# Kernel optimization log

Measured on AMD Instinct MI355X. Metric: run time of the kernel, lower is better.

Reference implementation:

```python
import jax, jax.numpy as jnp
import numpy as np

N, K, C, CL = 1024, 32, 64, 128
H = 2 * C  # MLP hidden = 2 * pair channels


def _ln(x, g, b, eps=1e-5):
    m = x.mean(-1, keepdims=True)
    v = jnp.mean(jnp.square(x - m), -1, keepdims=True)
    return (x - m) * jax.lax.rsqrt(v + eps) * g + b


def setup_inputs() -> dict:
    key = jax.random.key(0)
    ks = jax.random.split(key, 16)

    def w(k, shape):
        return jax.random.normal(k, shape, jnp.float32) / np.float32(np.sqrt(shape[0]))

    local = jax.random.normal(ks[0], (N, CL), jnp.float32)
    pair = jax.random.normal(ks[1], (N, N, C), jnp.float32)
    pair_update = jax.random.normal(ks[2], (N, K, C), jnp.float32)
    r = jax.random.randint(ks[3], (N, K), -(N // 4), N)
    neighbours = jnp.where(r < 0, -1, r)
    mask = jax.random.bernoulli(ks[4], 0.9, (N,))
    return dict(
        local=local, pair=pair, pair_update=pair_update,
        neighbours=neighbours, mask=mask,
        Wa=w(ks[5], (CL, C)), Wb=w(ks[6], (CL, C)),
        ln_g=jnp.ones((C,), jnp.float32), ln_b=jnp.zeros((C,), jnp.float32),
        W_aug=w(ks[7], (C, C)), W_lin=w(ks[8], (C, C)),
        W_left=w(ks[9], (C, 32)), b_left=jnp.zeros((32,), jnp.float32),
        W_right=w(ks[10], (C, 32)), b_right=jnp.zeros((32,), jnp.float32),
        W1=w(ks[11], (32, H)), W2=w(ks[12], (H, C)),
        W_int=w(ks[13], (CL, C)), b_int=jnp.zeros((C,), jnp.float32),
    )


def reference(local, pair, pair_update, neighbours, mask,
              Wa, Wb, ln_g, ln_b, W_aug, W_lin,
              W_left, b_left, W_right, b_right, W1, W2, W_int, b_int):
    idx = jnp.arange(pair.shape[0])
    # inject local info into the sparse pair update   [N,K,C]
    pu = pair_update + (local @ Wa)[:, None] + (local @ Wb)[neighbours]
    # gather neighbour pair features + layernorm      [N,K,C]
    lp = _ln(pair[idx[:, None], neighbours], ln_g, ln_b)
    lp = lp + pu @ W_aug
    linear = lp @ W_lin                               # [N,K,C]
    left = lp @ W_left + b_left                       # [N,K,32]
    right = lp @ W_right + b_right                    # [N,K,32]
    # neighbour-of-neighbour pair features            [N,K,K,32]
    npair = left[:, None] + right[neighbours]
    pn = neighbours[neighbours]                       # [N,K,K]
    pn = jnp.where((neighbours == -1)[:, :, None], pn, -1)
    pm = (pn != -1) & mask[pn] & (neighbours != -1)[:, None, :]
    # fused per-edge-pair MLP                          [N,K,K,C]
    upd = jax.nn.gelu(npair @ W1) @ W2
    # masked mean over the middle neighbour axis       [N,K,C]
    upd = jnp.where(pm[..., None], upd, 0.0).sum(axis=1)
    upd = upd / jnp.maximum(pm.sum(axis=1), 1).astype(upd.dtype)[..., None]
    inter = local @ W_int + b_int                     # [N,C]
    # scatter-add back into the dense pair tensor (collisions possible)
    return pair.at[idx[:, None], neighbours].add(upd + inter[:, None] + linear)
```

## Files before the change

### kernel.cpp

```cpp
#include <hip/hip_runtime.h>
#include <hip/hip_bf16.h>

constexpr int Nn  = 1024;
constexpr int Kk  = 32;
constexpr int Cc  = 64;
constexpr int CLl = 128;

typedef unsigned int   u32;
typedef unsigned short u16;

__device__ __forceinline__ float gelu_tanh(float v){
  float c = 0.7978845608028654f*(v + 0.044715f*v*v*v);
  return 0.5f*v*(1.f + tanhf(c));
}
__device__ __forceinline__ float bflo(u32 u){ return __uint_as_float(u<<16); }
__device__ __forceinline__ float bfhi(u32 u){ return __uint_as_float(u & 0xffff0000u); }
__device__ __forceinline__ u32 pack_bf(float a, float b){
  u32 xa = __float_as_uint(a), xb = __float_as_uint(b);
  u32 ra = (xa + 0x7fffu + ((xa>>16)&1u)) >> 16;
  u32 rb = (xb + 0x7fffu + ((xb>>16)&1u)) >> 16;
  return ra | (rb<<16);
}

__global__ __launch_bounds__(64) void k0(
    const float* __restrict__ local, const float* __restrict__ Wa,
    const float* __restrict__ Wb, const float* __restrict__ Wint,
    const float* __restrict__ b_int,
    float* __restrict__ A, float* __restrict__ B, float* __restrict__ inter){
  int i = blockIdx.x;
  int c = threadIdx.x;
  __shared__ float l[CLl];
  l[c]      = local[i*CLl + c];
  l[c + 64] = local[i*CLl + 64 + c];
  __syncthreads();
  float a = 0.f, b = 0.f, t = 0.f;
  #pragma unroll 4
  for(int d = 0; d < CLl; ++d){
    float ld = l[d];
    a = fmaf(ld, Wa[d*Cc + c], a);
    b = fmaf(ld, Wb[d*Cc + c], b);
    t = fmaf(ld, Wint[d*Cc + c], t);
  }
  A[i*Cc + c] = a;
  B[i*Cc + c] = b;
  inter[i*Cc + c] = t + b_int[c];
}

__global__ __launch_bounds__(256) void k1(
    const float* __restrict__ pair, const float* __restrict__ pair_update,
    const int* __restrict__ neigh, const int* __restrict__ mask,
    const float* __restrict__ ln_g, const float* __restrict__ ln_b,
    const float* __restrict__ W_aug, const float* __restrict__ W_right,
    const float* __restrict__ b_right,
    const float* __restrict__ A, const float* __restrict__ B,
    float* __restrict__ r1023, int* __restrict__ qpart){
  const int i = Nn - 1;
  __shared__ float wA[4096];
  __shared__ float wR[2048];
  __shared__ float p [Kk][68];
  __shared__ float pu[Kk][68];
  __shared__ float lp[Kk][68];
  __shared__ int   nwS[Kk];
  __shared__ float ssum[Kk][9], ssq[Kk][9], stats[Kk][2];
  int tid = threadIdx.x;
  for(int idx = tid; idx < 4096; idx += 256) wA[idx] = W_aug[idx];
  for(int idx = tid; idx < 2048; idx += 256) wR[idx] = W_right[idx];
  if(tid < Kk){
    int n = neigh[i*Kk + tid];
    nwS[tid] = (n < 0) ? n + Nn : n;
    qpart[tid] = (n != -1 && mask[n] != 0) ? 1 : 0;
  }
  __syncthreads();
  int k = tid >> 3, s = tid & 7;
  {
    const float* prow = pair + ((size_t)i*Nn + nwS[k])*Cc + s*8;
    const float* pur  = pair_update + ((size_t)i*Kk + k)*Cc + s*8;
    const float* Ar = A + i*Cc + s*8;
    const float* Br = B + (size_t)nwS[k]*Cc + s*8;
    float ps = 0.f, ps2 = 0.f;
    for(int j = 0; j < 8; ++j){
      float v = prow[j];
      p[k][s*8 + j] = v; ps += v; ps2 += v*v;
      pu[k][s*8 + j] = pur[j] + Ar[j] + Br[j];
    }
    ssum[k][s] = ps; ssq[k][s] = ps2;
  }
  __syncthreads();
  if(s == 0){
    float m = 0.f, q = 0.f;
    for(int j = 0; j < 8; ++j){ m += ssum[k][j]; q += ssq[k][j]; }
    m *= (1.f/64.f); q *= (1.f/64.f);
    float var = fmaxf(q - m*m, 0.f);
    stats[k][0] = m; stats[k][1] = rsqrtf(var + 1e-5f);
  }
  __syncthreads();
  {
    float m = stats[k][0], r = stats[k][1];
    float acc[8];
    #pragma unroll
    for(int j = 0; j < 8; ++j){
      int c = s*8 + j;
      acc[j] = (p[k][c] - m)*r*ln_g[c] + ln_b[c];
    }
    for(int d = 0; d < 64; ++d){
      float pd = pu[k][d];
      #pragma unroll
      for(int j = 0; j < 8; ++j) acc[j] = fmaf(pd, wA[d*64 + s*8 + j], acc[j]);
    }
    #pragma unroll
    for(int j = 0; j < 8; ++j) lp[k][s*8 + j] = acc[j];
  }
  __syncthreads();
  {
    float acc[4] = {0.f,0.f,0.f,0.f};
    for(int d = 0; d < 64; ++d){
      float ld = lp[k][d];
      #pragma unroll
      for(int j = 0; j < 4; ++j) acc[j] = fmaf(ld, wR[d*32 + s*4 + j], acc[j]);
    }
    #pragma unroll
    for(int j = 0; j < 4; ++j)
      r1023[k*32 + s*4 + j] = acc[j] + b_right[s*4 + j];
  }
}

__global__ __launch_bounds__(256) void k2a(
    const float* __restrict__ pair, const float* __restrict__ pair_update,
    const int* __restrict__ neigh,
    const float* __restrict__ ln_g, const float* __restrict__ ln_b,
    const float* __restrict__ W_aug, const float* __restrict__ W_lin,
    const float* __restrict__ W_left, const float* __restrict__ b_left,
    const float* __restrict__ A, const float* __restrict__ B,
    const float* __restrict__ inter, const float* __restrict__ r1023,
    float* __restrict__ hG, float* __restrict__ linG){
  __shared__ u32 wbA[2048];
  __shared__ u32 wbL[2048];
  __shared__ u32 wbF[1024];
  __shared__ float pbuf [Kk][68];
  __shared__ float pubuf[Kk][68];
  __shared__ float AiS[64], InS[64], lgS[64], lbS[64];
  __shared__ float ssum[Kk][9], ssq[Kk][9], stats[Kk][2];
  __shared__ int nwS[Kk];

  int i   = blockIdx.x;
  int tid = threadIdx.x;

  for(int idx = tid; idx < 2048; idx += 256){
    const float2 wa = *(const float2*)(W_aug + idx*2);
    wbA[idx] = pack_bf(wa.x, wa.y);
    const float2 wl = *(const float2*)(W_lin + idx*2);
    wbL[idx] = pack_bf(wl.x, wl.y);
  }
  for(int idx = tid; idx < 1024; idx += 256){
    const float2 wf = *(const float2*)(W_left + idx*2);
    wbF[idx] = pack_bf(wf.x, wf.y);
  }
  if(tid < Kk){
    int n = neigh[i*Kk + tid];
    nwS[tid] = (n < 0) ? n + Nn : n;
  }
  if(tid < 64){
    AiS[tid] = A[i*Cc + tid];
    InS[tid] = inter[i*Cc + tid];
    lgS[tid] = ln_g[tid];
    lbS[tid] = ln_b[tid];
  }
  __syncthreads();

  {
    int k8 = tid >> 3, s8 = tid & 7;
    const float4* p4 = (const float4*)(pair + ((size_t)i*Nn + nwS[k8])*Cc) + s8*2;
    float4 p0 = p4[0], p1 = p4[1];
    const float4* u4 = (const float4*)(pair_update + ((size_t)i*Kk + k8)*Cc) + s8*2;
    float4 u0 = u4[0], u1 = u4[1];
    const float4* Br = (const float4*)(B + (size_t)nwS[k8]*Cc) + s8*2;
    float4 b0 = Br[0], b1 = Br[1];
    float pf[8] = {p0.x,p0.y,p0.z,p0.w,p1.x,p1.y,p1.z,p1.w};
    float uf[8] = {u0.x,u0.y,u0.z,u0.w,u1.x,u1.y,u1.z,u1.w};
    float bv[8] = {b0.x,b0.y,b0.z,b0.w,b1.x,b1.y,b1.z,b1.w};
    float ps = 0.f, ps2 = 0.f;
    #pragma unroll
    for(int j = 0; j < 8; ++j){
      float v = pf[j];
      pbuf[k8][s8*8 + j] = v; ps += v; ps2 += v*v;
      pubuf[k8][s8*8 + j] = uf[j] + AiS[s8*8 + j] + bv[j];
    }
    ssum[k8][s8] = ps; ssq[k8][s8] = ps2;
  }
  __syncthreads();

  if((tid & 7) == 0){
    int k8 = tid >> 3;
    float m = 0.f, q = 0.f;
    for(int j = 0; j < 8; ++j){ m += ssum[k8][j]; q += ssq[k8][j]; }
    m *= (1.f/64.f); q *= (1.f/64.f);
    float var = fmaxf(q - m*m, 0.f);
    stats[k8][0] = m; stats[k8][1] = rsqrtf(var + 1e-5f);
  }
  __syncthreads();

  int kq = tid >> 4;
  int s  = tid & 15;
  int k0 = kq, k1i = kq + 16;
  int c0 = s*4;

  float a0[4], a1[4];
  {
    float m0 = stats[k0][0], r0 = stats[k0][1];
    float m1 = stats[k1i][0], r1 = stats[k1i][1];
    #pragma unroll
    for(int j = 0; j < 4; ++j){
      int c = c0 + j;
      a0[j] = (pbuf[k0][c]  - m0)*r0*lgS[c] + lbS[c];
      a1[j] = (pbuf[k1i][c] - m1)*r1*lgS[c] + lbS[c];
    }
    #pragma unroll 4
    for(int d = 0; d < 64; ++d){
      uint2 wv = *(const uint2*)&wbA[d*32 + s*2];
      float w0 = bflo(wv.x), w1 = bfhi(wv.x), w2 = bflo(wv.y), w3 = bfhi(wv.y);
      float p0 = pubuf[k0][d], p1 = pubuf[k1i][d];
      a0[0] = fmaf(p0, w0, a0[0]); a0[1] = fmaf(p0, w1, a0[1]);
      a0[2] = fmaf(p0, w2, a0[2]); a0[3] = fmaf(p0, w3, a0[3]);
      a1[0] = fmaf(p1, w0, a1[0]); a1[1] = fmaf(p1, w1, a1[1]);
      a1[2] = fmaf(p1, w2, a1[2]); a1[3] = fmaf(p1, w3, a1[3]);
    }
  }
  __syncthreads();
  {
    #pragma unroll
    for(int j = 0; j < 4; ++j){ pbuf[k0][c0 + j] = a0[j]; pbuf[k1i][c0 + j] = a1[j]; }
  }
  __syncthreads();

  {
    float L0[4] = {0,0,0,0}, L1[4] = {0,0,0,0};
    float X0[2] = {0,0},     X1[2] = {0,0};
    #pragma unroll 4
    for(int d = 0; d < 64; ++d){
      float p0 = pbuf[k0][d], p1 = pbuf[k1i][d];
      uint2 wv = *(const uint2*)&wbL[d*32 + s*2];
      float w0 = bflo(wv.x), w1 = bfhi(wv.x), w2 = bflo(wv.y), w3 = bfhi(wv.y);
      L0[0] = fmaf(p0, w0, L0[0]); L0[1] = fmaf(p0, w1, L0[1]);
      L0[2] = fmaf(p0, w2, L0[2]); L0[3] = fmaf(p0, w3, L0[3]);
      L1[0] = fmaf(p1, w0, L1[0]); L1[1] = fmaf(p1, w1, L1[1]);
      L1[2] = fmaf(p1, w2, L1[2]); L1[3] = fmaf(p1, w3, L1[3]);
      u32 wf = wbF[d*16 + s];
      float f0 = bflo(wf), f1 = bfhi(wf);
      X0[0] = fmaf(p0, f0, X0[0]); X0[1] = fmaf(p0, f1, X0[1]);
      X1[0] = fmaf(p1, f0, X1[0]); X1[1] = fmaf(p1, f1, X1[1]);
    }
    float4 o0 = make_float4(L0[0]+InS[c0], L0[1]+InS[c0+1], L0[2]+InS[c0+2], L0[3]+InS[c0+3]);
    float4 o1 = make_float4(L1[0]+InS[c0], L1[1]+InS[c0+1], L1[2]+InS[c0+2], L1[3]+InS[c0+3]);
    *(float4*)(linG + ((size_t)i*Kk + k0 )*Cc + c0) = o0;
    *(float4*)(linG + ((size_t)i*Kk + k1i)*Cc + c0) = o1;
    int x0 = s*2;
    float2 bl = *(const float2*)(b_left + x0);
    float2 rA = *(const float2*)(r1023 + k0*32  + x0);
    float2 rB = *(const float2*)(r1023 + k1i*32 + x0);
    float2 h0 = make_float2(X0[0] + bl.x + rA.x, X0[1] + bl.y + rA.y);
    float2 h1 = make_float2(X1[0] + bl.x + rB.x, X1[1] + bl.y + rB.y);
    *(float2*)(hG + ((size_t)i*Kk + k0 )*32 + x0) = h0;
    *(float2*)(hG + ((size_t)i*Kk + k1i)*32 + x0) = h1;
  }
}

__global__ __launch_bounds__(256) void kfuse(
    const float* __restrict__ pair, const int* __restrict__ neigh,
    const float* __restrict__ W1, const float* __restrict__ W2,
    const float* __restrict__ hG, const float* __restrict__ linG,
    const int* __restrict__ qpart,
    float* __restrict__ out){
  __shared__ u32 w1b[2048];
  __shared__ u32 w2b[4096];
  __shared__ float hbuf[Kk][36];
  __shared__ float cbuf[Kk][68];
  __shared__ int nbS[Kk], nwS[Kk], quS[Kk], leadS[Kk];
  __shared__ int cminus;

  int i   = blockIdx.x;
  int tid = threadIdx.x;

  {
    const float4* src = (const float4*)(pair + (size_t)i*Nn*Cc);
    float4*       dst = (float4*)(out + (size_t)i*Nn*Cc);
    #pragma unroll 4
    for(int idx = tid; idx < 16384; idx += 256) dst[idx] = src[idx];
  }

  for(int idx = tid; idx < 2048; idx += 256){
    const float2 w1 = *(const float2*)(W1 + idx*2);
    w1b[idx] = pack_bf(w1.x, w1.y);
    const float2 wa = *(const float2*)(W2 + idx*2);
    w2b[idx] = pack_bf(wa.x, wa.y);
    const float2 wb2 = *(const float2*)(W2 + 4096 + idx*2);
    w2b[2048 + idx] = pack_bf(wb2.x, wb2.y);
  }
  for(int idx = tid; idx < 1024; idx += 256)
    hbuf[idx >> 5][idx & 31] = hG[(size_t)i*1024 + idx];
  if(tid < Kk){
    int n = neigh[i*Kk + tid];
    nbS[tid] = n;
    nwS[tid] = (n < 0) ? n + Nn : n;
    quS[tid] = qpart[tid];
  }
  __syncthreads();
  if(tid == 0){
    int c = 0;
    for(int kk = 0; kk < Kk; ++kk) c |= (nbS[kk] == -1);
    cminus = c;
  }

  int kq = tid >> 4;
  int s  = tid & 15;

  float g0[8], g1v[8];
  {
    float A0[8], A1[8];
    #pragma unroll
    for(int j = 0; j < 8; ++j){ A0[j] = 0.f; A1[j] = 0.f; }
    #pragma unroll 2
    for(int x = 0; x < 32; ++x){
      float h0 = hbuf[kq][x], h1 = hbuf[kq+16][x];
      uint4 wv = *(const uint4*)&w1b[x*64 + s*4];
      float w[8] = {bflo(wv.x),bfhi(wv.x),bflo(wv.y),bfhi(wv.y),
                    bflo(wv.z),bfhi(wv.z),bflo(wv.w),bfhi(wv.w)};
      #pragma unroll
      for(int j = 0; j < 8; ++j){
        A0[j] = fmaf(h0, w[j], A0[j]);
        A1[j] = fmaf(h1, w[j], A1[j]);
      }
    }
    #pragma unroll
    for(int j = 0; j < 8; ++j){ g0[j] = gelu_tanh(A0[j]); g1v[j] = gelu_tanh(A1[j]); }
  }
  __syncthreads();

  {
    float V0[4] = {0,0,0,0}, V1[4] = {0,0,0,0};
    int lbase = (kq & 3) << 4;
    for(int hb = 0; hb < 16; ++hb){
      int src = lbase | hb;
      #pragma unroll
      for(int hj = 0; hj < 8; ++hj){
        float gA = __shfl(g0[hj],  src, 64);
        float gB = __shfl(g1v[hj], src, 64);
        int h = hb*8 + hj;
        uint2 wv = *(const uint2*)&w2b[h*32 + s*2];
        float w0 = bflo(wv.x), w1 = bfhi(wv.x), w2 = bflo(wv.y), w3 = bfhi(wv.y);
        V0[0] = fmaf(gA, w0, V0[0]); V0[1] = fmaf(gA, w1, V0[1]);
        V0[2] = fmaf(gA, w2, V0[2]); V0[3] = fmaf(gA, w3, V0[3]);
        V1[0] = fmaf(gB, w0, V1[0]); V1[1] = fmaf(gB, w1, V1[1]);
        V1[2] = fmaf(gB, w2, V1[2]); V1[3] = fmaf(gB, w3, V1[3]);
      }
    }
    int c0 = s*4;
    float4 l0 = *(const float4*)(linG + ((size_t)i*Kk + kq     )*Cc + c0);
    float4 l1 = *(const float4*)(linG + ((size_t)i*Kk + kq + 16)*Cc + c0);
    float mul0 = (cminus && quS[kq]      && nbS[kq]      != -1) ? 1.f : 0.f;
    float mul1 = (cminus && quS[kq + 16] && nbS[kq + 16] != -1) ? 1.f : 0.f;
    cbuf[kq][c0+0] = fmaf(mul0, V0[0], l0.x);
    cbuf[kq][c0+1] = fmaf(mul0, V0[1], l0.y);
    cbuf[kq][c0+2] = fmaf(mul0, V0[2], l0.z);
    cbuf[kq][c0+3] = fmaf(mul0, V0[3], l0.w);
    cbuf[kq+16][c0+0] = fmaf(mul1, V1[0], l1.x);
    cbuf[kq+16][c0+1] = fmaf(mul1, V1[1], l1.y);
    cbuf[kq+16][c0+2] = fmaf(mul1, V1[2], l1.z);
    cbuf[kq+16][c0+3] = fmaf(mul1, V1[3], l1.w);
  }
  __syncthreads();

  if(tid < Kk){
    int lead = 1;
    for(int kk = 0; kk < tid; ++kk) if(nwS[kk] == nwS[tid]) lead = 0;
    leadS[tid] = lead;
  }
  __syncthreads();
  {
    int k8 = tid >> 3, s8 = tid & 7;
    if(leadS[k8]){
      int col = nwS[k8];
      float tot[8] = {0,0,0,0,0,0,0,0};
      for(int kk = 0; kk < Kk; ++kk){
        if(nwS[kk] == col){
          #pragma unroll
          for(int j = 0; j < 8; ++j) tot[j] += cbuf[kk][s8*8 + j];
        }
      }
      size_t base = ((size_t)i*Nn + col)*Cc + s8*8;
      const float4* pv = (const float4*)(pair + base);
      float4 p0 = pv[0], p1 = pv[1];
      float4 o0 = make_float4(p0.x+tot[0], p0.y+tot[1], p0.z+tot[2], p0.w+tot[3]);
      float4 o1 = make_float4(p1.x+tot[4], p1.y+tot[5], p1.z+tot[6], p1.w+tot[7]);
      float4* ov = (float4*)(out + base);
      ov[0] = o0; ov[1] = o1;
    }
  }
}

extern "C" void kernel_launch(void* const* d_in, const int* in_sizes, int n_in,
                              void* d_out, int out_size, void* d_ws, size_t ws_size,
                              hipStream_t stream){
  (void)in_sizes; (void)n_in; (void)out_size; (void)ws_size;
  const float* local       = (const float*)d_in[0];
  const float* pair        = (const float*)d_in[1];
  const float* pair_update = (const float*)d_in[2];
  const int*   neighbours  = (const int*)d_in[3];
  const int*   mask        = (const int*)d_in[4];
  const float* Wa          = (const float*)d_in[5];
  const float* Wb          = (const float*)d_in[6];
  const float* ln_g        = (const float*)d_in[7];
  const float* ln_b        = (const float*)d_in[8];
  const float* W_aug       = (const float*)d_in[9];
  const float* W_lin       = (const float*)d_in[10];
  const float* W_left      = (const float*)d_in[11];
  const float* b_left      = (const float*)d_in[12];
  const float* W_right     = (const float*)d_in[13];
  const float* b_right     = (const float*)d_in[14];
  const float* W1          = (const float*)d_in[15];
  const float* W2          = (const float*)d_in[16];
  const float* W_int       = (const float*)d_in[17];
  const float* b_int       = (const float*)d_in[18];

  float* ws    = (float*)d_ws;
  float* A     = ws;
  float* B     = ws + 65536;
  float* inter = ws + 131072;
  float* r1023 = ws + 196608;
  int*   qpart = (int*)(ws + 197632);
  float* hG    = ws + 197664;
  float* linG  = ws + 1246240;

  k0<<<dim3(Nn), dim3(64), 0, stream>>>(local, Wa, Wb, W_int, b_int, A, B, inter);
  k1<<<dim3(1), dim3(256), 0, stream>>>(pair, pair_update, neighbours, mask,
                                        ln_g, ln_b, W_aug, W_right, b_right,
                                        A, B, r1023, qpart);
  k2a<<<dim3(Nn), dim3(256), 0, stream>>>(pair, pair_update, neighbours,
                                          ln_g, ln_b, W_aug, W_lin, W_left, b_left,
                                          A, B, inter, r1023, hG, linG);
  kfuse<<<dim3(Nn), dim3(256), 0, stream>>>(pair, neighbours, W1, W2, hG, linG,
                                            qpart, (float*)d_out);
}
```

Baseline: 548.7 us.

## Fuse k2a and kfuse into one kernel with interleaved row copy

Merges the per-row projection kernel and the MLP/scatter kernel into a single kernel, keeping h and linear in registers and shared memory instead of passing them through global workspace buffers. The dense pair-to-out row copy is split into three chunks placed between compute phases so memory traffic can overlap with arithmetic. The pair_update sum is also stored as packed bf16 in shared memory. Shared-memory use rises, which can lower occupancy, and the bf16 packing of the input activation adds precision loss.

```diff
diff --git a/kernel.cpp b/kernel.cpp
--- a/kernel.cpp
+++ b/kernel.cpp
@@ -8,6 +8,7 @@
 
 typedef unsigned int   u32;
 typedef unsigned short u16;
+typedef float f4v __attribute__((ext_vector_type(4)));
 
 __device__ __forceinline__ float gelu_tanh(float v){
   float c = 0.7978845608028654f*(v + 0.044715f*v*v*v);
@@ -124,32 +125,58 @@
   }
 }
 
-__global__ __launch_bounds__(256) void k2a(
+__global__ __launch_bounds__(256) void kbig(
     const float* __restrict__ pair, const float* __restrict__ pair_update,
     const int* __restrict__ neigh,
     const float* __restrict__ ln_g, const float* __restrict__ ln_b,
     const float* __restrict__ W_aug, const float* __restrict__ W_lin,
     const float* __restrict__ W_left, const float* __restrict__ b_left,
+    const float* __restrict__ W1, const float* __restrict__ W2,
     const float* __restrict__ A, const float* __restrict__ B,
     const float* __restrict__ inter, const float* __restrict__ r1023,
-    float* __restrict__ hG, float* __restrict__ linG){
+    const int* __restrict__ qpart,
+    float* __restrict__ out){
+
   __shared__ u32 wbA[2048];
   __shared__ u32 wbL[2048];
   __shared__ u32 wbF[1024];
-  __shared__ float pbuf [Kk][68];
-  __shared__ float pubuf[Kk][68];
+  __shared__ u32 w1b[2048];
+  __shared__ u32 w2b[4096];
+  __shared__ float pbuf[Kk][68];
+  __shared__ u32  puP [Kk][34];
+  __shared__ float uA[1088];
+  __shared__ float stats[Kk][2];
   __shared__ float AiS[64], InS[64], lgS[64], lbS[64];
-  __shared__ float ssum[Kk][9], ssq[Kk][9], stats[Kk][2];
-  __shared__ int nwS[Kk];
-
-  int i   = blockIdx.x;
-  int tid = threadIdx.x;
+  __shared__ int nbS[Kk], nwS[Kk], quS[Kk], leadS[Kk];
+  __shared__ int cminus;
+
+  float* ssum = uA;
+  float* ssq  = uA + 288;
+  float* hbuf = uA;
+
+  const int i   = blockIdx.x;
+  const int tid = threadIdx.x;
+
+  const f4v* __restrict__ srcRow = (const f4v*)(pair + (size_t)i*Nn*Cc);
+  f4v* __restrict__       dstRow = (f4v*)(out + (size_t)i*Nn*Cc);
+
+  #pragma unroll 4
+  for(int it = 0; it < 32; ++it){
+    int idx = it*256 + tid;
+    dstRow[idx] = srcRow[idx];
+  }
 
   for(int idx = tid; idx < 2048; idx += 256){
     const float2 wa = *(const float2*)(W_aug + idx*2);
     wbA[idx] = pack_bf(wa.x, wa.y);
     const float2 wl = *(const float2*)(W_lin + idx*2);
     wbL[idx] = pack_bf(wl.x, wl.y);
+    const float2 w1 = *(const float2*)(W1 + idx*2);
+    w1b[idx] = pack_bf(w1.x, w1.y);
+    const float2 w2a = *(const float2*)(W2 + idx*2);
+    w2b[idx] = pack_bf(w2a.x, w2a.y);
+    const float2 w2c = *(const float2*)(W2 + 4096 + idx*2);
+    w2b[2048 + idx] = pack_bf(w2c.x, w2c.y);
   }
   for(int idx = tid; idx < 1024; idx += 256){
     const float2 wf = *(const float2*)(W_left + idx*2);
@@ -157,7 +184,9 @@
   }
   if(tid < Kk){
     int n = neigh[i*Kk + tid];
+    nbS[tid] = n;
     nwS[tid] = (n < 0) ? n + Nn : n;
+    quS[tid] = qpart[tid];
   }
   if(tid < 64){
     AiS[tid] = A[i*Cc + tid];
@@ -166,6 +195,17 @@
     lbS[tid] = ln_b[tid];
   }
   __syncthreads();
+
+  if(tid == 0){
+    int c = 0;
+    for(int kk = 0; kk < Kk; ++kk) c |= (nbS[kk] == -1);
+    cminus = c;
+  }
+  if(tid < Kk){
+    int lead = 1;
+    for(int kk = 0; kk < tid; ++kk) if(nwS[kk] == nwS[tid]) lead = 0;
+    leadS[tid] = lead;
+  }
 
   {
     int k8 = tid >> 3, s8 = tid & 7;
@@ -183,144 +223,117 @@
     for(int j = 0; j < 8; ++j){
       float v = pf[j];
       pbuf[k8][s8*8 + j] = v; ps += v; ps2 += v*v;
-      pubuf[k8][s8*8 + j] = uf[j] + AiS[s8*8 + j] + bv[j];
-    }
-    ssum[k8][s8] = ps; ssq[k8][s8] = ps2;
+    }
+    #pragma unroll
+    for(int j = 0; j < 4; ++j){
+      float e0 = uf[2*j]   + AiS[s8*8 + 2*j]   + bv[2*j];
+      float e1 = uf[2*j+1] + AiS[s8*8 + 2*j+1] + bv[2*j+1];
+      puP[k8][s8*4 + j] = pack_bf(e0, e1);
+    }
+    ssum[k8*9 + s8] = ps; ssq[k8*9 + s8] = ps2;
   }
   __syncthreads();
 
   if((tid & 7) == 0){
     int k8 = tid >> 3;
     float m = 0.f, q = 0.f;
-    for(int j = 0; j < 8; ++j){ m += ssum[k8][j]; q += ssq[k8][j]; }
+    for(int j = 0; j < 8; ++j){ m += ssum[k8*9 + j]; q += ssq[k8*9 + j]; }
     m *= (1.f/64.f); q *= (1.f/64.f);
     float var = fmaxf(q - m*m, 0.f);
     stats[k8][0] = m; stats[k8][1] = rsqrtf(var + 1e-5f);
   }
   __syncthreads();
 
-  int kq = tid >> 4;
-  int s  = tid & 15;
-  int k0 = kq, k1i = kq + 16;
-  int c0 = s*4;
+  const int kq  = tid >> 4;
+  const int s   = tid & 15;
+  const int k0i = kq, k1i = kq + 16;
+  const int c0  = s*4;
 
   float a0[4], a1[4];
   {
-    float m0 = stats[k0][0], r0 = stats[k0][1];
+    float m0 = stats[k0i][0], r0 = stats[k0i][1];
     float m1 = stats[k1i][0], r1 = stats[k1i][1];
     #pragma unroll
     for(int j = 0; j < 4; ++j){
       int c = c0 + j;
-      a0[j] = (pbuf[k0][c]  - m0)*r0*lgS[c] + lbS[c];
+      a0[j] = (pbuf[k0i][c] - m0)*r0*lgS[c] + lbS[c];
       a1[j] = (pbuf[k1i][c] - m1)*r1*lgS[c] + lbS[c];
     }
+    #pragma unroll 2
+    for(int dp = 0; dp < 32; ++dp){
+      u32 q0 = puP[k0i][dp], q1 = puP[k1i][dp];
+      float pe0 = bflo(q0), po0 = bfhi(q0);
+      float pe1 = bflo(q1), po1 = bfhi(q1);
+      uint2 we = *(const uint2*)&wbA[(2*dp)*32 + s*2];
+      uint2 wo = *(const uint2*)&wbA[(2*dp+1)*32 + s*2];
+      float w0 = bflo(we.x), w1 = bfhi(we.x), w2 = bflo(we.y), w3 = bfhi(we.y);
+      a0[0] = fmaf(pe0, w0, a0[0]); a0[1] = fmaf(pe0, w1, a0[1]);
+      a0[2] = fmaf(pe0, w2, a0[2]); a0[3] = fmaf(pe0, w3, a0[3]);
+      a1[0] = fmaf(pe1, w0, a1[0]); a1[1] = fmaf(pe1, w1, a1[1]);
+      a1[2] = fmaf(pe1, w2, a1[2]); a1[3] = fmaf(pe1, w3, a1[3]);
+      float x0w = bflo(wo.x), x1w = bfhi(wo.x), x2w = bflo(wo.y), x3w = bfhi(wo.y);
+      a0[0] = fmaf(po0, x0w, a0[0]); a0[1] = fmaf(po0, x1w, a0[1]);
+      a0[2] = fmaf(po0, x2w, a0[2]); a0[3] = fmaf(po0, x3w, a0[3]);
+      a1[0] = fmaf(po1, x0w, a1[0]); a1[1] = fmaf(po1, x1w, a1[1]);
+      a1[2] = fmaf(po1, x2w, a1[2]); a1[3] = fmaf(po1, x3w, a1[3]);
+    }
+  }
+  __syncthreads();
+  #pragma unroll
+  for(int j = 0; j < 4; ++j){ pbuf[k0i][c0 + j] = a0[j]; pbuf[k1i][c0 + j] = a1[j]; }
+
+  #pragma unroll 4
+  for(int it = 32; it < 48; ++it){
+    int idx = it*256 + tid;
+    dstRow[idx] = srcRow[idx];
+  }
+  __syncthreads();
+
+  float L0[4], L1[4];
+  {
+    float Lx0[4] = {0,0,0,0}, Lx1[4] = {0,0,0,0};
+    float X0[2] = {0,0}, X1[2] = {0,0};
     #pragma unroll 4
     for(int d = 0; d < 64; ++d){
-      uint2 wv = *(const uint2*)&wbA[d*32 + s*2];
-      float w0 = bflo(wv.x), w1 = bfhi(wv.x), w2 = bflo(wv.y), w3 = bfhi(wv.y);
-      float p0 = pubuf[k0][d], p1 = pubuf[k1i][d];
-      a0[0] = fmaf(p0, w0, a0[0]); a0[1] = fmaf(p0, w1, a0[1]);
-      a0[2] = fmaf(p0, w2, a0[2]); a0[3] = fmaf(p0, w3, a0[3]);
-      a1[0] = fmaf(p1, w0, a1[0]); a1[1] = fmaf(p1, w1, a1[1]);
-      a1[2] = fmaf(p1, w2, a1[2]); a1[3] = fmaf(p1, w3, a1[3]);
-    }
-  }
-  __syncthreads();
-  {
-    #pragma unroll
-    for(int j = 0; j < 4; ++j){ pbuf[k0][c0 + j] = a0[j]; pbuf[k1i][c0 + j] = a1[j]; }
-  }
-  __syncthreads();
-
-  {
-    float L0[4] = {0,0,0,0}, L1[4] = {0,0,0,0};
-    float X0[2] = {0,0},     X1[2] = {0,0};
-    #pragma unroll 4
-    for(int d = 0; d < 64; ++d){
-      float p0 = pbuf[k0][d], p1 = pbuf[k1i][d];
+      float p0 = pbuf[k0i][d], p1 = pbuf[k1i][d];
       uint2 wv = *(const uint2*)&wbL[d*32 + s*2];
       float w0 = bflo(wv.x), w1 = bfhi(wv.x), w2 = bflo(wv.y), w3 = bfhi(wv.y);
-      L0[0] = fmaf(p0, w0, L0[0]); L0[1] = fmaf(p0, w1, L0[1]);
-      L0[2] = fmaf(p0, w2, L0[2]); L0[3] = fmaf(p0, w3, L0[3]);
-      L1[0] = fmaf(p1, w0, L1[0]); L1[1] = fmaf(p1, w1, L1[1]);
-      L1[2] = fmaf(p1, w2, L1[2]); L1[3] = fmaf(p1, w3, L1[3]);
+      Lx0[0] = fmaf(p0, w0, Lx0[0]); Lx0[1] = fmaf(p0, w1, Lx0[1]);
+      Lx0[2] = fmaf(p0, w2, Lx0[2]); Lx0[3] = fmaf(p0, w3, Lx0[3]);
+      Lx1[0] = fmaf(p1, w0, Lx1[0]); Lx1[1] = fmaf(p1, w1, Lx1[1]);
+      Lx1[2] = fmaf(p1, w2, Lx1[2]); Lx1[3] = fmaf(p1, w3, Lx1[3]);
       u32 wf = wbF[d*16 + s];
       float f0 = bflo(wf), f1 = bfhi(wf);
       X0[0] = fmaf(p0, f0, X0[0]); X0[1] = fmaf(p0, f1, X0[1]);
       X1[0] = fmaf(p1, f0, X1[0]); X1[1] = fmaf(p1, f1, X1[1]);
     }
-    float4 o0 = make_float4(L0[0]+InS[c0], L0[1]+InS[c0+1], L0[2]+InS[c0+2], L0[3]+InS[c0+3]);
-    float4 o1 = make_float4(L1[0]+InS[c0], L1[1]+InS[c0+1], L1[2]+InS[c0+2], L1[3]+InS[c0+3]);
-    *(float4*)(linG + ((size_t)i*Kk + k0 )*Cc + c0) = o0;
-    *(float4*)(linG + ((size_t)i*Kk + k1i)*Cc + c0) = o1;
+    #pragma unroll
+    for(int j = 0; j < 4; ++j){
+      L0[j] = Lx0[j] + InS[c0 + j];
+      L1[j] = Lx1[j] + InS[c0 + j];
+    }
     int x0 = s*2;
     float2 bl = *(const float2*)(b_left + x0);
-    float2 rA = *(const float2*)(r1023 + k0*32  + x0);
+    float2 rA = *(const float2*)(r1023 + k0i*32 + x0);
     float2 rB = *(const float2*)(r1023 + k1i*32 + x0);
-    float2 h0 = make_float2(X0[0] + bl.x + rA.x, X0[1] + bl.y + rA.y);
-    float2 h1 = make_float2(X1[0] + bl.x + rB.x, X1[1] + bl.y + rB.y);
-    *(float2*)(hG + ((size_t)i*Kk + k0 )*32 + x0) = h0;
-    *(float2*)(hG + ((size_t)i*Kk + k1i)*32 + x0) = h1;
-  }
-}
-
-__global__ __launch_bounds__(256) void kfuse(
-    const float* __restrict__ pair, const int* __restrict__ neigh,
-    const float* __restrict__ W1, const float* __restrict__ W2,
-    const float* __restrict__ hG, const float* __restrict__ linG,
-    const int* __restrict__ qpart,
-    float* __restrict__ out){
-  __shared__ u32 w1b[2048];
-  __shared__ u32 w2b[4096];
-  __shared__ float hbuf[Kk][36];
-  __shared__ float cbuf[Kk][68];
-  __shared__ int nbS[Kk], nwS[Kk], quS[Kk], leadS[Kk];
-  __shared__ int cminus;
-
-  int i   = blockIdx.x;
-  int tid = threadIdx.x;
-
-  {
-    const float4* src = (const float4*)(pair + (size_t)i*Nn*Cc);
-    float4*       dst = (float4*)(out + (size_t)i*Nn*Cc);
-    #pragma unroll 4
-    for(int idx = tid; idx < 16384; idx += 256) dst[idx] = src[idx];
-  }
-
-  for(int idx = tid; idx < 2048; idx += 256){
-    const float2 w1 = *(const float2*)(W1 + idx*2);
-    w1b[idx] = pack_bf(w1.x, w1.y);
-    const float2 wa = *(const float2*)(W2 + idx*2);
-    w2b[idx] = pack_bf(wa.x, wa.y);
-    const float2 wb2 = *(const float2*)(W2 + 4096 + idx*2);
-    w2b[2048 + idx] = pack_bf(wb2.x, wb2.y);
-  }
-  for(int idx = tid; idx < 1024; idx += 256)
-    hbuf[idx >> 5][idx & 31] = hG[(size_t)i*1024 + idx];
-  if(tid < Kk){
-    int n = neigh[i*Kk + tid];
-    nbS[tid] = n;
-    nwS[tid] = (n < 0) ? n + Nn : n;
-    quS[tid] = qpart[tid];
-  }
-  __syncthreads();
-  if(tid == 0){
-    int c = 0;
-    for(int kk = 0; kk < Kk; ++kk) c |= (nbS[kk] == -1);
-    cminus = c;
-  }
-
-  int kq = tid >> 4;
-  int s  = tid & 15;
+    hbuf[k0i*34 + x0]     = X0[0] + bl.x + rA.x;
+    hbuf[k0i*34 + x0 + 1] = X0[1] + bl.y + rA.y;
+    hbuf[k1i*34 + x0]     = X1[0] + bl.x + rB.x;
+    hbuf[k1i*34 + x0 + 1] = X1[1] + bl.y + rB.y;
+  }
+  #pragma unroll 4
+  for(int it = 48; it < 64; ++it){
+    int idx = it*256 + tid;
+    dstRow[idx] = srcRow[idx];
+  }
+  __syncthreads();
 
   float g0[8], g1v[8];
   {
-    float A0[8], A1[8];
-    #pragma unroll
-    for(int j = 0; j < 8; ++j){ A0[j] = 0.f; A1[j] = 0.f; }
+    float A0[8] = {0,0,0,0,0,0,0,0}, A1[8] = {0,0,0,0,0,0,0,0};
     #pragma unroll 2
     for(int x = 0; x < 32; ++x){
-      float h0 = hbuf[kq][x], h1 = hbuf[kq+16][x];
+      float h0 = hbuf[k0i*34 + x], h1 = hbuf[k1i*34 + x];
       uint4 wv = *(const uint4*)&w1b[x*64 + s*4];
       float w[8] = {bflo(wv.x),bfhi(wv.x),bflo(wv.y),bfhi(wv.y),
                     bflo(wv.z),bfhi(wv.z),bflo(wv.w),bfhi(wv.w)};
@@ -333,17 +346,15 @@
     #pragma unroll
     for(int j = 0; j < 8; ++j){ g0[j] = gelu_tanh(A0[j]); g1v[j] = gelu_tanh(A1[j]); }
   }
-  __syncthreads();
-
   {
     float V0[4] = {0,0,0,0}, V1[4] = {0,0,0,0};
     int lbase = (kq & 3) << 4;
     for(int hb = 0; hb < 16; ++hb){
-      int src = lbase | hb;
+      int srcl = lbase | hb;
       #pragma unroll
       for(int hj = 0; hj < 8; ++hj){
-        float gA = __shfl(g0[hj],  src, 64);
-        float gB = __shfl(g1v[hj], src, 64);
+        float gA = __shfl(g0[hj],  srcl, 64);
+        float gB = __shfl(g1v[hj], srcl, 64);
         int h = hb*8 + hj;
         uint2 wv = *(const uint2*)&w2b[h*32 + s*2];
         float w0 = bflo(wv.x), w1 = bfhi(wv.x), w2 = bflo(wv.y), w3 = bfhi(wv.y);
@@ -353,28 +364,16 @@
         V1[2] = fmaf(gB, w2, V1[2]); V1[3] = fmaf(gB, w3, V1[3]);
       }
     }
-    int c0 = s*4;
-    float4 l0 = *(const float4*)(linG + ((size_t)i*Kk + kq     )*Cc + c0);
-    float4 l1 = *(const float4*)(linG + ((size_t)i*Kk + kq + 16)*Cc + c0);
-    float mul0 = (cminus && quS[kq]      && nbS[kq]      != -1) ? 1.f : 0.f;
-    float mul1 = (cminus && quS[kq + 16] && nbS[kq + 16] != -1) ? 1.f : 0.f;
-    cbuf[kq][c0+0] = fmaf(mul0, V0[0], l0.x);
-    cbuf[kq][c0+1] = fmaf(mul0, V0[1], l0.y);
-    cbuf[kq][c0+2] = fmaf(mul0, V0[2], l0.z);
-    cbuf[kq][c0+3] = fmaf(mul0, V0[3], l0.w);
-    cbuf[kq+16][c0+0] = fmaf(mul1, V1[0], l1.x);
-    cbuf[kq+16][c0+1] = fmaf(mul1, V1[1], l1.y);
-    cbuf[kq+16][c0+2] = fmaf(mul1, V1[2], l1.z);
-    cbuf[kq+16][c0+3] = fmaf(mul1, V1[3], l1.w);
-  }
-  __syncthreads();
-
-  if(tid < Kk){
-    int lead = 1;
-    for(int kk = 0; kk < tid; ++kk) if(nwS[kk] == nwS[tid]) lead = 0;
-    leadS[tid] = lead;
-  }
-  __syncthreads();
+    float mul0 = (cminus && quS[k0i] && nbS[k0i] != -1) ? 1.f : 0.f;
+    float mul1 = (cminus && quS[k1i] && nbS[k1i] != -1) ? 1.f : 0.f;
+    #pragma unroll
+    for(int j = 0; j < 4; ++j){
+      pbuf[k0i][c0 + j] = fmaf(mul0, V0[j], L0[j]);
+      pbuf[k1i][c0 + j] = fmaf(mul1, V1[j], L1[j]);
+    }
+  }
+  __syncthreads();
+
   {
     int k8 = tid >> 3, s8 = tid & 7;
     if(leadS[k8]){
@@ -383,7 +382,7 @@
       for(int kk = 0; kk < Kk; ++kk){
         if(nwS[kk] == col){
           #pragma unroll
-          for(int j = 0; j < 8; ++j) tot[j] += cbuf[kk][s8*8 + j];
+          for(int j = 0; j < 8; ++j) tot[j] += pbuf[kk][s8*8 + j];
         }
       }
       size_t base = ((size_t)i*Nn + col)*Cc + s8*8;
@@ -427,16 +426,14 @@
   float* inter = ws + 131072;
   float* r1023 = ws + 196608;
   int*   qpart = (int*)(ws + 197632);
-  float* hG    = ws + 197664;
-  float* linG  = ws + 1246240;
 
   k0<<<dim3(Nn), dim3(64), 0, stream>>>(local, Wa, Wb, W_int, b_int, A, B, inter);
   k1<<<dim3(1), dim3(256), 0, stream>>>(pair, pair_update, neighbours, mask,
                                         ln_g, ln_b, W_aug, W_right, b_right,
                                         A, B, r1023, qpart);
-  k2a<<<dim3(Nn), dim3(256), 0, stream>>>(pair, pair_update, neighbours,
-                                          ln_g, ln_b, W_aug, W_lin, W_left, b_left,
-                                          A, B, inter, r1023, hG, linG);
-  kfuse<<<dim3(Nn), dim3(256), 0, stream>>>(pair, neighbours, W1, W2, hG, linG,
-                                            qpart, (float*)d_out);
-}
+  kbig<<<dim3(Nn), dim3(256), 0, stream>>>(pair, pair_update, neighbours,
+                                           ln_g, ln_b, W_aug, W_lin,
+                                           W_left, b_left, W1, W2,
+                                           A, B, inter, r1023, qpart,
+                                           (float*)d_out);
+}
```

Result: faster. 526.5 us (-4.0%).
